# Optimization experiments

Measured on AMD Instinct MI355X. Metric: run time of the kernel, lower is better.

## Reference

```python
import jax, jax.numpy as jnp
import numpy as np
from jax import lax

Z_MAX = 0.3
WAVELENGTHS = jnp.array([0.65, 0.53, 0.47], jnp.float32)
LUMA = jnp.array([0.299, 0.587, 0.114], jnp.float32)


def conv2d(x, w, b):
    # x: (B,C,H,W), w: (O,I,kh,kw), SAME padding, stride 1
    y = lax.conv_general_dilated(x, w, (1, 1), 'SAME',
                                 dimension_numbers=('NCHW', 'OIHW', 'NCHW'))
    return y + b[None, :, None, None]


def group_norm(x, g, b, eps=1e-5):
    # GroupNorm(num_groups=1): normalize over (C,H,W) per sample
    mu = x.mean(axis=(1, 2, 3), keepdims=True)
    var = ((x - mu) ** 2).mean(axis=(1, 2, 3), keepdims=True)
    xn = (x - mu) * lax.rsqrt(var + eps)
    return xn * g[None, :, None, None] + b[None, :, None, None]


def setup_inputs() -> dict:
    key = jax.random.key(0)
    ks = jax.random.split(key, 16)
    B, C, H, W = 8, 3, 512, 512
    PH, ZH, MH = 16, 16, 32
    s = 0.1
    inp = {
        'x': jax.random.uniform(ks[0], (B, C, H, W), jnp.float32),
        'norm_g': jnp.ones((C,), jnp.float32), 'norm_b': jnp.zeros((C,), jnp.float32),
        'ph_w1': jax.random.normal(ks[1], (PH, C, 3, 3), jnp.float32) * s,
        'ph_b1': jnp.zeros((PH,), jnp.float32),
        'ph_w2': jax.random.normal(ks[2], (C, PH, 3, 3), jnp.float32) * s,
        'ph_b2': jnp.zeros((C,), jnp.float32),
        'z_w1': jax.random.normal(ks[3], (ZH, C, 3, 3), jnp.float32) * s,
        'z_b1': jnp.zeros((ZH,), jnp.float32),
        'z_w2': jax.random.normal(ks[4], (C, ZH, 3, 3), jnp.float32) * s,
        'z_b2': jnp.zeros((C,), jnp.float32),
        'freq_gain': jax.random.normal(ks[5], (C,), jnp.float32) * 0.01,
        'mix_w1': jax.random.normal(ks[6], (MH, C + 2, 3, 3), jnp.float32) * s,
        'mix_b1': jnp.zeros((MH,), jnp.float32),
        'gn1_g': jnp.ones((MH,), jnp.float32), 'gn1_b': jnp.zeros((MH,), jnp.float32),
        'mix_w2': jax.random.normal(ks[7], (MH, MH, 3, 3), jnp.float32) * s,
        'mix_b2': jnp.zeros((MH,), jnp.float32),
        'gn2_g': jnp.ones((MH,), jnp.float32), 'gn2_b': jnp.zeros((MH,), jnp.float32),
        'mix_w3': jax.random.normal(ks[8], (C, MH, 1, 1), jnp.float32) * s,
        'mix_b3': jnp.zeros((C,), jnp.float32),
        'se_w1': jax.random.normal(ks[9], (4, C), jnp.float32) * s,   # mid = max(3//4,4)=4
        'se_b1': jnp.zeros((4,), jnp.float32),
        'se_w2': jax.random.normal(ks[10], (C, 4), jnp.float32) * s,
        'se_b2': jnp.zeros((C,), jnp.float32),
        'alpha': jnp.asarray(0.3, jnp.float32),
    }
    return inp


def reference(x, norm_g, norm_b, ph_w1, ph_b1, ph_w2, ph_b2,
              z_w1, z_b1, z_w2, z_b2, freq_gain,
              mix_w1, mix_b1, gn1_g, gn1_b, mix_w2, mix_b2, gn2_g, gn2_b,
              mix_w3, mix_b3, se_w1, se_b1, se_w2, se_b2, alpha):
    B, C, H, W = x.shape
    # 1) norm
    xn = group_norm(x, norm_g, norm_b)
    # 2) phase prediction (small CNN, phi in [-pi, pi])
    h = jax.nn.silu(conv2d(xn, ph_w1, ph_b1))
    phi = jnp.tanh(conv2d(h, ph_w2, ph_b2)) * jnp.pi
    # 3) per-pixel propagation distance z in [0, z_max]
    hz = jax.nn.silu(conv2d(xn, z_w1, z_b1))
    z = jax.nn.sigmoid(conv2d(hz, z_w2, z_b2)) * Z_MAX
    # 4) complex field U0 = amp * exp(i*phi)  (amp_mode='identity')
    U0 = lax.complex(x * jnp.cos(phi), x * jnp.sin(phi))
    # 5) ASM propagation. kz = 2*pi*sqrt(1/lam^2 - fx^2 - fy^2), per-channel wavelength.
    fy = jnp.fft.fftfreq(H).astype(jnp.float32)
    fx = jnp.fft.fftfreq(W).astype(jnp.float32)
    f2 = fy[:, None] ** 2 + fx[None, :] ** 2                     # (H,W)
    inv_l2 = (1.0 / WAVELENGTHS ** 2)[:, None, None]             # (3,1,1)
    kz = 2.0 * jnp.pi * jnp.sqrt(jnp.maximum(inv_l2 - f2[None], 0.0))  # (3,H,W)
    # spatially varying z: base propagation at mean z + spatial phase correction
    z_mean = z.mean(axis=(2, 3), keepdims=True)                  # (B,3,1,1)
    Uf = jnp.fft.fft2(U0)
    Uf = Uf * (1.0 + freq_gain)[None, :, None, None].astype(Uf.dtype)  # FreqEnhance gain
    hp = kz[None] * z_mean                                       # (B,3,H,W)
    Uz = jnp.fft.ifft2(Uf * lax.complex(jnp.cos(hp), jnp.sin(hp)))
    k0 = (2.0 * jnp.pi / WAVELENGTHS)[None, :, None, None]
    cp = k0 * (z - z_mean)
    Uz = Uz * lax.complex(jnp.cos(cp), jnp.sin(cp))
    # 6) J = |Uz| with clamped sqrt
    J = jnp.sqrt(jnp.maximum(Uz.real ** 2 + Uz.imag ** 2, 1e-12))
    # 7) mix head: [x, J_luma, J_contrast] -> delta
    lw = LUMA[None, :, None, None]
    x_l = (x * lw).sum(axis=1, keepdims=True)
    J_l = (J * lw).sum(axis=1, keepdims=True)
    mix_in = jnp.concatenate([x, J_l, J_l - x_l], axis=1)        # (B,5,H,W)
    d = jax.nn.silu(group_norm(conv2d(mix_in, mix_w1, mix_b1), gn1_g, gn1_b))
    d = jax.nn.silu(group_norm(conv2d(d, mix_w2, mix_b2), gn2_g, gn2_b))
    delta = conv2d(d, mix_w3, mix_b3)                            # (B,3,H,W)
    # 8) SE channel attention
    p = delta.mean(axis=(2, 3))                                  # (B,3)
    wse = jax.nn.sigmoid(jax.nn.silu(p @ se_w1.T + se_b1) @ se_w2.T + se_b2)
    delta = delta * wse[:, :, None, None]
    # 9) residual update
    return x + alpha * delta
```

## Files before the change

kernel.cpp:

```cpp
#include <hip/hip_runtime.h>
#include <hip/hip_bf16.h>
#include <math.h>

#define DINL __device__ __forceinline__

namespace {
constexpr int Bn = 8, Cn = 3, Hn = 512, Wn = 512;
constexpr int HW  = Hn * Wn;
constexpr int CHW = Cn * HW;
constexpr float GEPS = 1e-5f;
constexpr float PIf  = 3.14159265358979323846f;

constexpr size_t OFF_RED = 0;
constexpr size_t OFF_PHI = 512;
constexpr size_t OFF_U   = OFF_PHI + (size_t)Bn * CHW * 2;
constexpr size_t OFF_J   = OFF_U   + (size_t)Bn * CHW * 4;
constexpr size_t OFF_D   = OFF_J   + (size_t)Bn * CHW * 2;
constexpr size_t OFF_Y2  = OFF_D   + (size_t)Bn * CHW * 2;
constexpr size_t OFF_W1B = OFF_Y2  + (size_t)Bn * 32 * HW;
constexpr size_t OFF_W2F = OFF_W1B + 3072 * 2;
constexpr size_t OFF_WH1 = OFF_W2F + 9216;
constexpr size_t OFF_WP2 = OFF_WH1 + 4608 * 2;
constexpr size_t OFF_WZ2 = OFF_WP2 + 4608;
constexpr size_t OFF_PRM = OFF_WZ2 + 4608;
constexpr size_t OFF_PART= OFF_PRM + 160 * 4;
constexpr int PZ = 0;
constexpr int PG1 = 24576;
constexpr int PG2 = 40960;
constexpr int PD  = 57344;
}

typedef __bf16 bfx8 __attribute__((ext_vector_type(8)));
typedef float  fx4  __attribute__((ext_vector_type(4)));

DINL float frcp(float a) { return __builtin_amdgcn_rcpf(a); }
DINL float sigm(float a) { return frcp(1.f + __expf(-a)); }
DINL float siluf(float a) { return a * frcp(1.f + __expf(-a)); }
DINL float ftanh(float a) { return 1.f - 2.f * frcp(1.f + __expf(2.f * a)); }
DINL unsigned short f2bf(float f) {
    unsigned u = __float_as_uint(f);
    return (unsigned short)((u + 0x7FFFu + ((u >> 16) & 1u)) >> 16);
}
DINL float bf2f(unsigned short h) {
    return __uint_as_float(((unsigned)h) << 16);
}
DINL unsigned short t1(float a) { return (unsigned short)(__float_as_uint(a) >> 16); }
DINL unsigned t2(float a, float b) {
    return (__float_as_uint(a) >> 16) | (__float_as_uint(b) & 0xFFFF0000u);
}
DINL unsigned char f2f8(float v) {
    return (unsigned char)(__builtin_amdgcn_cvt_pk_fp8_f32(v, v, 0, false) & 0xFF);
}
DINL unsigned short pk8(float a, float b) {
    return (unsigned short)(__builtin_amdgcn_cvt_pk_fp8_f32(a, b, 0, false) & 0xFFFF);
}
template<int SEL>
DINL float f8f(unsigned u) { return __builtin_amdgcn_cvt_f32_fp8(u, SEL); }
DINL unsigned pkh(float a, float b) {
    auto h = __builtin_amdgcn_cvt_pkrtz(a, b);
    unsigned u; __builtin_memcpy(&u, &h, 4); return u;
}
DINL float2 uph(unsigned u) {
    _Float16 h[2]; __builtin_memcpy(h, &u, 4);
    return make_float2((float)h[0], (float)h[1]);
}
DINL unsigned short f2h(float a) {
    _Float16 h = (_Float16)a; unsigned short s; __builtin_memcpy(&s, &h, 2); return s;
}
DINL float h2f(unsigned short s) {
    _Float16 h; __builtin_memcpy(&h, &s, 2); return (float)h;
}

DINL float blockReduceSum(float v) {
    __shared__ float sm[4];
    int lane = threadIdx.x & 63, wid = threadIdx.x >> 6;
    #pragma unroll
    for (int o = 32; o > 0; o >>= 1) v += __shfl_down(v, o, 64);
    __syncthreads();
    if (lane == 0) sm[wid] = v;
    __syncthreads();
    if (wid == 0) {
        float r = (lane < 4) ? sm[lane] : 0.f;
        r += __shfl_down(r, 2, 64);
        r += __shfl_down(r, 1, 64);
        return r;
    }
    return 0.f;
}

__global__ void k_zero(float* __restrict__ red) { red[threadIdx.x] = 0.f; }

__global__ __launch_bounds__(256) void k_red(const float* __restrict__ src,
                                             float* __restrict__ dst)
{
    const float4* s4 = (const float4*)(src + (size_t)blockIdx.x * 1024);
    float4 q = s4[threadIdx.x];
    float r = blockReduceSum(q.x + q.y + q.z + q.w);
    if (threadIdx.x == 0) dst[blockIdx.x] = r;
}

__global__ __launch_bounds__(256) void k_prep(
    const float* __restrict__ w1, const float* __restrict__ w2,
    const float* __restrict__ phw1, const float* __restrict__ zw1,
    const float* __restrict__ phw2, const float* __restrict__ zw2,
    const float* __restrict__ g2g, const float* __restrict__ g2b,
    const float* __restrict__ w3,
    unsigned short* __restrict__ w1bf, unsigned char* __restrict__ w2f8,
    unsigned short* __restrict__ wh1, unsigned char* __restrict__ wp2,
    unsigned char* __restrict__ wz2, float* __restrict__ prm)
{
    int i = blockIdx.x * 256 + threadIdx.x;
    if (i < 3072) {
        int o = i / 96, k = i - o * 96;
        int ky = k >> 5, r = k & 31, kx = r >> 3, c = r & 7;
        float v = (kx < 3 && c < 5) ? w1[o * 45 + c * 9 + ky * 3 + kx] : 0.f;
        w1bf[i] = f2bf(v);
    }
    if (i < 9216) {
        int tap = i >> 10, rr = i & 1023, o = rr >> 5, ci = rr & 31;
        w2f8[i] = f2f8(w2[o * 288 + ci * 9 + tap]);
    }
    if (i < 4608) {
        int o = i / 96, k = i - o * 96;
        int ky = k >> 5, r = k & 31, kx = r >> 3, c = r & 7;
        float v = 0.f;
        if (kx < 3 && c < 3)
            v = (o < 16) ? phw1[o * 27 + c * 9 + ky * 3 + kx]
                         : zw1[(o - 16) * 27 + c * 9 + ky * 3 + kx];
        wh1[i] = f2bf(v);
    }
    if (i < 4608) {
        int tap = i / 512, rr = i - tap * 512, n = rr >> 5, k = rr & 31;
        float vp = (n < 3 && k < 16) ? phw2[n * 144 + k * 9 + tap] : 0.f;
        float vz = (n < 3) ? zw2[n * 288 + k * 9 + tap] : 0.f;
        wp2[i] = f2f8(vp);
        wz2[i] = f2f8(vz);
    }
    if (i < 160) {
        if (i < 32) {
            int ch = (i & 1) * 16 + (i >> 1);
            prm[i] = g2g[ch];
        } else if (i < 64) {
            int j = i - 32, ch = (j & 1) * 16 + (j >> 1);
            prm[i] = g2b[ch];
        } else {
            int j = (i - 64) & 31, c = (i - 64) >> 5;
            int ch = (j & 1) * 16 + (j >> 1);
            prm[i] = w3[c * 32 + ch];
        }
    }
}

__global__ __launch_bounds__(256) void k_reduce_x(const float* __restrict__ x,
                                                  float* __restrict__ red) {
    int b = blockIdx.x >> 5, blk = blockIdx.x & 31;
    const float4* xv = (const float4*)(x + (size_t)b * CHW + (size_t)blk * (CHW / 32));
    float s = 0.f, ss = 0.f;
    for (int i = threadIdx.x; i < (CHW / 32) / 4; i += 256) {
        float4 v = xv[i];
        s  += v.x + v.y + v.z + v.w;
        ss += v.x * v.x + v.y * v.y + v.z * v.z + v.w * v.w;
    }
    float rs = blockReduceSum(s);
    float rss = blockReduceSum(ss);
    if (threadIdx.x == 0) { atomicAdd(&red[b], rs); atomicAdd(&red[8 + b], rss); }
}

__global__ __launch_bounds__(256) void k_heads(
    const float* __restrict__ x, const float* __restrict__ red,
    const float* __restrict__ ng, const float* __restrict__ nb,
    const unsigned short* __restrict__ wh1,
    const float* __restrict__ phb1, const float* __restrict__ zb1,
    const unsigned char* __restrict__ wp2, const unsigned char* __restrict__ wz2,
    const float* __restrict__ phb2, const float* __restrict__ zb2,
    unsigned short* __restrict__ phi, float* __restrict__ part)
{
    const int tx0 = blockIdx.x * 16, ty0 = blockIdx.y * 16, b = blockIdx.z;
    const int local = blockIdx.y * 32 + blockIdx.x;
    const bool edge = (blockIdx.x == 0) || (blockIdx.x == 31) ||
                      (blockIdx.y == 0) || (blockIdx.y == 31);
    __shared__ unsigned short mt8[20 * 21 * 8];
    __shared__ __attribute__((aligned(16))) unsigned char ht8[324 * 48];
    const int t = threadIdx.x;
    const float mu = red[b] * (1.f / CHW);
    const float rsv = rsqrtf(red[8 + b] * (1.f / CHW) - mu * mu + GEPS);
    float sc[3], sh[3];
    #pragma unroll
    for (int c = 0; c < 3; ++c) { sc[c] = rsv * ng[c]; sh[c] = nb[c] - mu * rsv * ng[c]; }
    if (edge) {
        for (int e = t; e < 20 * 21; e += 256) {
            int yy = e / 21, xx = e - yy * 21;
            int gy = ty0 - 2 + yy, gx = tx0 - 2 + xx;
            float v0 = 0, v1 = 0, v2 = 0;
            if (xx < 20 && (unsigned)gy < (unsigned)Hn && (unsigned)gx < (unsigned)Wn) {
                size_t p = (size_t)b * CHW + (size_t)gy * Wn + gx;
                v0 = x[p] * sc[0] + sh[0];
                v1 = x[p + HW] * sc[1] + sh[1];
                v2 = x[p + 2 * HW] * sc[2] + sh[2];
            }
            *(uint4*)(mt8 + e * 8) = make_uint4(t2(v0, v1), (unsigned)t1(v2), 0u, 0u);
        }
    } else {
        for (int e = t; e < 20 * 21; e += 256) {
            int yy = e / 21, xx = e - yy * 21;
            float v0 = 0, v1 = 0, v2 = 0;
            if (xx < 20) {
                size_t p = (size_t)b * CHW + (size_t)(ty0 - 2 + yy) * Wn + (tx0 - 2 + xx);
                v0 = x[p] * sc[0] + sh[0];
                v1 = x[p + HW] * sc[1] + sh[1];
                v2 = x[p + 2 * HW] * sc[2] + sh[2];
            }
            *(uint4*)(mt8 + e * 8) = make_uint4(t2(v0, v1), (unsigned)t1(v2), 0u, 0u);
        }
    }
    const int wv = t >> 6, lane = t & 63, ln = lane & 15, q = lane >> 4;
    bfx8 Bf[3][3];
    #pragma unroll
    for (int ks = 0; ks < 3; ++ks)
        #pragma unroll
        for (int nt = 0; nt < 3; ++nt)
            Bf[ks][nt] = *(const bfx8*)(wh1 + (nt * 16 + ln) * 96 + ks * 32 + q * 8);
    const float bb0 = phb1[ln], bb1 = zb1[ln], bb2 = zb1[16 + ln];
    __syncthreads();
    for (int mt = wv; mt < 21; mt += 4) {
        int p = mt * 16 + ln; if (p > 323) p = 323;
        const int hy = p / 18, hx = p - hy * 18;
        fx4 a0 = {0,0,0,0}, a1 = {0,0,0,0}, a2 = {0,0,0,0};
        #pragma unroll
        for (int ks = 0; ks < 3; ++ks) {
            bfx8 A = *(const bfx8*)(mt8 + ((hy + ks) * 21 + hx + q) * 8);
            a0 = __builtin_amdgcn_mfma_f32_16x16x32_bf16(A, Bf[ks][0], a0, 0, 0, 0);
            a1 = __builtin_amdgcn_mfma_f32_16x16x32_bf16(A, Bf[ks][1], a1, 0, 0, 0);
            a2 = __builtin_amdgcn_mfma_f32_16x16x32_bf16(A, Bf[ks][2], a2, 0, 0, 0);
        }
        const int prb = mt * 16 + q * 4;
        if (edge) {
            #pragma unroll
            for (int r = 0; r < 4; ++r) {
                const int pr = prb + r;
                if (pr < 324) {
                    const int py = pr / 18, px = pr - py * 18;
                    const int gy = ty0 - 1 + py, gx = tx0 - 1 + px;
                    const bool inimg = (unsigned)gy < (unsigned)Hn && (unsigned)gx < (unsigned)Wn;
                    unsigned char* hp = ht8 + pr * 48;
                    hp[ln]      = inimg ? f2f8(siluf(a0[r] + bb0)) : (unsigned char)0;
                    hp[16 + ln] = inimg ? f2f8(siluf(a1[r] + bb1)) : (unsigned char)0;
                    hp[32 + ln] = inimg ? f2f8(siluf(a2[r] + bb2)) : (unsigned char)0;
                }
            }
        } else {
            #pragma unroll
            for (int r = 0; r < 4; ++r) {
                const int pr = prb + r;
                if (pr < 324) {
                    unsigned char* hp = ht8 + pr * 48;
                    hp[ln]      = f2f8(siluf(a0[r] + bb0));
                    hp[16 + ln] = f2f8(siluf(a1[r] + bb1));
                    hp[32 + ln] = f2f8(siluf(a2[r] + bb2));
                }
            }
        }
    }
    __syncthreads();
    fx4 accp[4], accz[4];
    #pragma unroll
    for (int i = 0; i < 4; ++i) { accp[i] = fx4{0,0,0,0}; accz[i] = fx4{0,0,0,0}; }
    #pragma unroll
    for (int tap = 0; tap < 9; ++tap) {
        const int ky = tap / 3, kx = tap - ky * 3;
        long Bp = *(const long*)(wp2 + tap * 512 + ln * 32 + q * 8);
        long Bz = *(const long*)(wz2 + tap * 512 + ln * 32 + q * 8);
        #pragma unroll
        for (int i = 0; i < 4; ++i) {
            const int oy = wv * 4 + i;
            const unsigned char* ap = ht8 + ((oy + ky) * 18 + ln + kx) * 48;
            long Ap = *(const long*)(ap + q * 8);
            long Az = *(const long*)(ap + 16 + q * 8);
            accp[i] = __builtin_amdgcn_mfma_f32_16x16x32_fp8_fp8(Ap, Bp, accp[i], 0, 0, 0);
            accz[i] = __builtin_amdgcn_mfma_f32_16x16x32_fp8_fp8(Az, Bz, accz[i], 0, 0, 0);
        }
    }
    __syncthreads();
    float* phs = (float*)ht8;
    float* zs  = phs + 1024;
    if (ln < 3) {
        #pragma unroll
        for (int i = 0; i < 4; ++i)
            #pragma unroll
            for (int r = 0; r < 4; ++r) {
                int pl = (wv * 4 + i) * 16 + q * 4 + r;
                phs[pl * 4 + ln] = accp[i][r];
                zs [pl * 4 + ln] = accz[i][r];
            }
    }
    asm volatile("" ::: "memory");
    float4 pv = ((const float4*)phs)[t];
    float4 zv = ((const float4*)zs)[t];
    const int gy = ty0 + (t >> 4), gx = tx0 + (t & 15);
    size_t pp = (size_t)b * CHW + (size_t)gy * Wn + gx;
    phi[pp]          = f2h(ftanh(pv.x + phb2[0]) * PIf);
    phi[pp + HW]     = f2h(ftanh(pv.y + phb2[1]) * PIf);
    phi[pp + 2 * HW] = f2h(ftanh(pv.z + phb2[2]) * PIf);
    float z0 = sigm(zv.x + zb2[0]) * 0.3f;
    float z1 = sigm(zv.y + zb2[1]) * 0.3f;
    float z2 = sigm(zv.z + zb2[2]) * 0.3f;
    float r0 = blockReduceSum(z0);
    float r1 = blockReduceSum(z1);
    float r2 = blockReduceSum(z2);
    if (t == 0) {
        part[PZ + (size_t)(b * 3 + 0) * 1024 + local] = r0;
        part[PZ + (size_t)(b * 3 + 1) * 1024 + local] = r1;
        part[PZ + (size_t)(b * 3 + 2) * 1024 + local] = r2;
    }
}

template<bool INV>
DINL float2* fft512_wave4(float2* a, float2* b, const float2* tw, int l)
{
    float2* src = a; float2* dst = b;
    int s = 1;
    #pragma unroll
    for (int st = 0; st < 4; ++st) {
        #pragma unroll
        for (int h = 0; h < 2; ++h) {
            const int i = l + h * 64;
            const int q = i & (s - 1);
            const int sm = i - q;
            float2 A = src[i], B = src[i + 128], C = src[i + 256], D = src[i + 384];
            float t0x = A.x + C.x, t0y = A.y + C.y;
            float t1x = A.x - C.x, t1y = A.y - C.y;
            float t2x = B.x + D.x, t2y = B.y + D.y;
            float t3x = B.x - D.x, t3y = B.y - D.y;
            float i3x = INV ? -t3y : t3y;
            float i3y = INV ? t3x : -t3x;
            float u0x = t0x + t2x, u0y = t0y + t2y;
            float u2x = t0x - t2x, u2y = t0y - t2y;
            float u1x = t1x + i3x, u1y = t1y + i3y;
            float u3x = t1x - i3x, u3y = t1y - i3y;
            float2 w1 = tw[sm], w2 = tw[2 * sm], w3 = tw[3 * sm];
            float w1y = INV ? -w1.y : w1.y;
            float w2y = INV ? -w2.y : w2.y;
            float w3y = INV ? -w3.y : w3.y;
            const int base = q + 4 * sm;
            dst[base]         = make_float2(u0x, u0y);
            dst[base + s]     = make_float2(u1x * w1.x - u1y * w1y, u1x * w1y + u1y * w1.x);
// ... 57 lines not shown
    __shared__ unsigned ta[32][33];
    __shared__ unsigned tb[32][33];
    const int t = threadIdx.x;
    const int cc = t & 31, r0 = t >> 5;
    const int ar = ti * 32, ac = tj * 32;
    #pragma unroll
    for (int k = 0; k < 4; ++k) {
        int r = r0 + k * 8;
        ta[r][cc] = Ub[(size_t)(ar + r) * 512 + ac + cc];
    }
    if (ti != tj) {
        #pragma unroll
        for (int k = 0; k < 4; ++k) {
            int r = r0 + k * 8;
            tb[r][cc] = Ub[(size_t)(ac + r) * 512 + ar + cc];
        }
    }
    __syncthreads();
    #pragma unroll
    for (int k = 0; k < 4; ++k) {
        int r = r0 + k * 8;
        Ub[(size_t)(ac + r) * 512 + ar + cc] = ta[cc][r];
    }
    if (ti != tj) {
        #pragma unroll
        for (int k = 0; k < 4; ++k) {
            int r = r0 + k * 8;
            Ub[(size_t)(ar + r) * 512 + ac + cc] = tb[cc][r];
        }
    }
}

__global__ __launch_bounds__(256) void k_fftB(
    unsigned* __restrict__ U, const float* __restrict__ red, const float* __restrict__ fgain)
{
    __shared__ float2 buf[4][2][512];
    __shared__ float2 tw[512];
    const int t = threadIdx.x, wv = t >> 6, l = t & 63;
    #pragma unroll
    for (int i = t; i < 512; i += 256) {
        float s, c; __sincosf(-2.f * PIf * (float)i * (1.f / 512.f), &s, &c);
        tw[i] = make_float2(c, s);
    }
    __syncthreads();
    const int line = blockIdx.x * 4 + wv;
    const int bc = line >> 9;
    const int fw = line & 511;
    const int c = bc % 3;
    unsigned* Ur = U + (size_t)line * 512;
    float2* A = buf[wv][0];
    float2* B = buf[wv][1];
    #pragma unroll
    for (int i = l; i < 512; i += 64) A[i] = uph(Ur[i]);
    asm volatile("" ::: "memory");
    float2* res = fft512_wave4<false>(A, B, tw, l);
    const float zm   = red[16 + bc] * (1.f / HW);
    const float gain = 1.f + fgain[c];
    const float lam  = (c == 0) ? 0.65f : (c == 1) ? 0.53f : 0.47f;
    const float il2  = 1.f / (lam * lam);
    const float fwv  = (float)(fw < 256 ? fw : fw - 512) * (1.f / 512.f);
    const float f2w  = fwv * fwv;
    #pragma unroll
    for (int i = l; i < 512; i += 64) {
        float fh = (float)(i < 256 ? i : i - 512) * (1.f / 512.f);
        float kz = 2.f * PIf * sqrtf(fmaxf(il2 - f2w - fh * fh, 0.f));
        float sn, cs; __sincosf(kz * zm, &sn, &cs);
        float2 v = res[i];
        res[i] = make_float2(gain * (v.x * cs - v.y * sn), gain * (v.x * sn + v.y * cs));
    }
    asm volatile("" ::: "memory");
    float2* other = (res == A) ? B : A;
    float2* res2 = fft512_wave4<true>(res, other, tw, l);
    #pragma unroll
    for (int i = l; i < 512; i += 64) {
        float2 v = res2[i];
        Ur[i] = pkh(v.x * (1.f / 512.f), v.y * (1.f / 512.f));
    }
}

__global__ __launch_bounds__(256) void k_fftC(
    const unsigned* __restrict__ U, unsigned short* __restrict__ J)
{
    __shared__ float2 buf[4][2][512];
    __shared__ float2 tw[512];
    const int t = threadIdx.x, wv = t >> 6, l = t & 63;
    #pragma unroll
    for (int i = t; i < 512; i += 256) {
        float s, c; __sincosf(-2.f * PIf * (float)i * (1.f / 512.f), &s, &c);
        tw[i] = make_float2(c, s);
// ... 52 lines not shown
        for (int nt = 0; nt < 2; ++nt)
            Bf[ks][nt] = *(const bfx8*)(w1bf + (nt * 16 + ln) * 96 + ks * 32 + q * 8);
    const float b1v0 = b1[ln], b1v1 = b1[16 + ln];
    float s = 0.f, ss = 0.f;
    #pragma unroll
    for (int i = 0; i < 4; ++i) {
        const int oy = wv * 4 + i;
        fx4 a0 = {0.f, 0.f, 0.f, 0.f}, a1 = {0.f, 0.f, 0.f, 0.f};
        #pragma unroll
        for (int ks = 0; ks < 3; ++ks) {
            bfx8 A = *(const bfx8*)(mt8 + ((oy + ks) * 19 + ln + q) * 8);
            a0 = __builtin_amdgcn_mfma_f32_16x16x32_bf16(A, Bf[ks][0], a0, 0, 0, 0);
            a1 = __builtin_amdgcn_mfma_f32_16x16x32_bf16(A, Bf[ks][1], a1, 0, 0, 0);
        }
        #pragma unroll
        for (int r = 0; r < 4; ++r) {
            float u0 = a0[r] + b1v0, u1 = a1[r] + b1v1;
            s += u0 + u1; ss += u0 * u0 + u1 * u1;
        }
    }
    float rs = blockReduceSum(s);
    float rss = blockReduceSum(ss);
    if (t == 0) {
        part[PG1 + (size_t)b * 1024 + local] = rs;
        part[PG1 + (size_t)(8 + b) * 1024 + local] = rss;
    }
}

__global__ __launch_bounds__(256) void k_m2(
    const float* __restrict__ x, const unsigned short* __restrict__ Jb,
    const unsigned short* __restrict__ w1bf, const float* __restrict__ b1,
    const float* __restrict__ g1g, const float* __restrict__ g1b,
    const unsigned char* __restrict__ w2f8, const float* __restrict__ b2,
    const float* __restrict__ red, float* __restrict__ part,
    unsigned char* __restrict__ y2)
{
    const int tx0 = blockIdx.x * 16, ty0 = blockIdx.y * 16, b = blockIdx.z;
    const int local = blockIdx.y * 32 + blockIdx.x;
    const bool edge = (blockIdx.x == 0) || (blockIdx.x == 31) ||
                      (blockIdx.y == 0) || (blockIdx.y == 31);
    __shared__ unsigned short mt8[20 * 21 * 8];
    __shared__ __attribute__((aligned(16))) unsigned char dt2[324 * 40];
    const int t = threadIdx.x;
    const float mu1 = red[40 + b] * (1.f / (32.f * HW));
    const float rs1 = rsqrtf(red[48 + b] * (1.f / (32.f * HW)) - mu1 * mu1 + GEPS);
    for (int e = t; e < 20 * 21; e += 256) {
        int yy = e / 21, xx = e - yy * 21;
        int gy = ty0 - 2 + yy, gx = tx0 - 2 + xx;
        float v0 = 0, v1 = 0, v2 = 0, jl = 0, d5 = 0;
        bool ok = edge ? (xx < 20 && (unsigned)gy < (unsigned)Hn && (unsigned)gx < (unsigned)Wn)
                       : (xx < 20);
        if (ok) {
            size_t p = (size_t)b * CHW + (size_t)gy * Wn + gx;
            v0 = x[p]; v1 = x[p + HW]; v2 = x[p + 2 * HW];
            float j0 = h2f(Jb[p]), j1 = h2f(Jb[p + HW]), j2 = h2f(Jb[p + 2 * HW]);
            float xl = 0.299f * v0 + 0.587f * v1 + 0.114f * v2;
            jl = 0.299f * j0 + 0.587f * j1 + 0.114f * j2;
            d5 = jl - xl;
        }
        *(uint4*)(mt8 + e * 8) = make_uint4(t2(v0, v1), t2(v2, jl), (unsigned)t1(d5), 0u);
    }
    const int wv = t >> 6, lane = t & 63, ln = lane & 15, q = lane >> 4;
    const float sc0 = rs1 * g1g[ln],       sc1 = rs1 * g1g[16 + ln];
    const float of0 = (b1[ln] - mu1) * sc0 + g1b[ln];
    const float of1 = (b1[16 + ln] - mu1) * sc1 + g1b[16 + ln];
    bfx8 Bf[3][2];
    #pragma unroll
    for (int ks = 0; ks < 3; ++ks)
        #pragma unroll
        for (int nt = 0; nt < 2; ++nt)
            Bf[ks][nt] = *(const bfx8*)(w1bf + (nt * 16 + ln) * 96 + ks * 32 + q * 8);
    __syncthreads();
    for (int mt = wv; mt < 21; mt += 4) {
        int p = mt * 16 + ln; if (p > 323) p = 323;
        const int hy = p / 18, hx = p - hy * 18;
        fx4 a0 = {0.f, 0.f, 0.f, 0.f}, a1 = {0.f, 0.f, 0.f, 0.f};
        #pragma unroll
        for (int ks = 0; ks < 3; ++ks) {
            bfx8 A = *(const bfx8*)(mt8 + ((hy + ks) * 21 + hx + q) * 8);
            a0 = __builtin_amdgcn_mfma_f32_16x16x32_bf16(A, Bf[ks][0], a0, 0, 0, 0);
            a1 = __builtin_amdgcn_mfma_f32_16x16x32_bf16(A, Bf[ks][1], a1, 0, 0, 0);
        }
        const int prb = mt * 16 + q * 4;
        if (edge) {
            #pragma unroll
            for (int r = 0; r < 4; ++r) {
                const int pr = prb + r;
                if (pr < 324) {
                    const int py = pr / 18, px = pr - py * 18;
                    const int gy = ty0 - 1 + py, gx = tx0 - 1 + px;
                    const bool inimg = (unsigned)gy < (unsigned)Hn && (unsigned)gx < (unsigned)Wn;
                    dt2[pr * 40 + ln]      = inimg ? f2f8(siluf(a0[r] * sc0 + of0)) : (unsigned char)0;
                    dt2[pr * 40 + 16 + ln] = inimg ? f2f8(siluf(a1[r] * sc1 + of1)) : (unsigned char)0;
                }
            }
        } else {
            #pragma unroll
            for (int r = 0; r < 4; ++r) {
                const int pr = prb + r;
                if (pr < 324) {
                    dt2[pr * 40 + ln]      = f2f8(siluf(a0[r] * sc0 + of0));
                    dt2[pr * 40 + 16 + ln] = f2f8(siluf(a1[r] * sc1 + of1));
                }
            }
        }
    }
    __syncthreads();
    fx4 c2[4][2];
    #pragma unroll
    for (int i = 0; i < 4; ++i)
        #pragma unroll
        for (int nt = 0; nt < 2; ++nt)
            c2[i][nt] = fx4{0.f, 0.f, 0.f, 0.f};
    #pragma unroll
    for (int tap = 0; tap < 9; ++tap) {
        const int ky = tap / 3, kx = tap - ky * 3;
        long B0 = *(const long*)(w2f8 + tap * 1024 + ln * 32 + q * 8);
        long B1 = *(const long*)(w2f8 + tap * 1024 + (16 + ln) * 32 + q * 8);
        #pragma unroll
        for (int i = 0; i < 4; ++i) {
            const int oy = wv * 4 + i;
            long A = *(const long*)(dt2 + ((oy + ky) * 18 + ln + kx) * 40 + q * 8);
            c2[i][0] = __builtin_amdgcn_mfma_f32_16x16x32_fp8_fp8(A, B0, c2[i][0], 0, 0, 0);
            c2[i][1] = __builtin_amdgcn_mfma_f32_16x16x32_fp8_fp8(A, B1, c2[i][1], 0, 0, 0);
        }
    }
    float s = 0.f, ss = 0.f;
    const float b2v0 = b2[ln], b2v1 = b2[16 + ln];
    #pragma unroll
    for (int i = 0; i < 4; ++i) {
        const int gy = ty0 + wv * 4 + i;
        #pragma unroll
        for (int r = 0; r < 4; ++r) {
            const int gx = tx0 + q * 4 + r;
            float a0 = c2[i][0][r] + b2v0;
            float a1 = c2[i][1][r] + b2v1;
            s += a0 + a1; ss += a0 * a0 + a1 * a1;
            size_t off = ((size_t)b * HW + (size_t)gy * Wn + gx) * 32 + ln * 2;
            *(unsigned short*)(y2 + off) = pk8(a0, a1);
        }
    }
    float rsum = blockReduceSum(s);
    float rss = blockReduceSum(ss);
    if (t == 0) {
        part[PG2 + (size_t)b * 1024 + local] = rsum;
        part[PG2 + (size_t)(8 + b) * 1024 + local] = rss;
    }
}

__global__ __launch_bounds__(256) void k_m3(
    const unsigned char* __restrict__ y2, const float* __restrict__ red,
    const float* __restrict__ prm, const float* __restrict__ b3,
    unsigned short* __restrict__ dl, float* __restrict__ part)
{
    int idx = blockIdx.x * 256 + threadIdx.x;
    int b = idx >> 18;
    int pix = idx & (HW - 1);
    const int local = blockIdx.x & 1023;
    float mu = red[56 + b] * (1.f / (32.f * HW));
    float rs = rsqrtf(red[64 + b] * (1.f / (32.f * HW)) - mu * mu + GEPS);
    const uint4* yp = (const uint4*)(y2 + (size_t)idx * 32);
    uint4 L0 = yp[0], L1 = yp[1];
    unsigned Lw[8] = {L0.x, L0.y, L0.z, L0.w, L1.x, L1.y, L1.z, L1.w};
    float a0 = b3[0], a1 = b3[1], a2 = b3[2];
    #pragma unroll
    for (int w = 0; w < 8; ++w) {
        unsigned u = Lw[w];
        float vv[4] = { f8f<0>(u), f8f<1>(u), f8f<2>(u), f8f<3>(u) };
        #pragma unroll
        for (int h = 0; h < 4; ++h) {
            int j = w * 4 + h;
            float dn = (vv[h] - mu) * rs * prm[j] + prm[32 + j];
            float sv = siluf(dn);
            a0 += sv * prm[64 + j]; a1 += sv * prm[96 + j]; a2 += sv * prm[128 + j];
        }
    }
    size_t p = (size_t)b * CHW + pix;
    dl[p] = f2h(a0); dl[p + HW] = f2h(a1); dl[p + 2 * HW] = f2h(a2);
    float r0 = blockReduceSum(a0);
    float r1 = blockReduceSum(a1);
    float r2 = blockReduceSum(a2);
    if (threadIdx.x == 0) {
        part[PD + (size_t)(b * 3 + 0) * 1024 + local] = r0;
        part[PD + (size_t)(b * 3 + 1) * 1024 + local] = r1;
        part[PD + (size_t)(b * 3 + 2) * 1024 + local] = r2;
    }
}

__global__ void k_se(float* __restrict__ red,
    const float* __restrict__ w1, const float* __restrict__ b1,
    const float* __restrict__ w2, const float* __restrict__ b2,
    const float* __restrict__ alpha)
{
    int b = threadIdx.x;
    if (b < 8) {
        float p0 = red[72 + b * 3 + 0] * (1.f / HW);
        float p1 = red[72 + b * 3 + 1] * (1.f / HW);
        float p2 = red[72 + b * 3 + 2] * (1.f / HW);
        float h[4];
        #pragma unroll
        for (int j = 0; j < 4; ++j) {
            float a = b1[j] + p0 * w1[j * 3] + p1 * w1[j * 3 + 1] + p2 * w1[j * 3 + 2];
            h[j] = siluf(a);
        }
        float al = alpha[0];
        #pragma unroll
        for (int c = 0; c < 3; ++c) {
            float a = b2[c] + h[0] * w2[c * 4] + h[1] * w2[c * 4 + 1]
                            + h[2] * w2[c * 4 + 2] + h[3] * w2[c * 4 + 3];
            red[96 + b * 3 + c] = al * sigm(a);
        }
    }
}

__global__ __launch_bounds__(256) void k_out(
    const float* __restrict__ x, const unsigned short* __restrict__ dl,
    const float* __restrict__ red, float* __restrict__ out)
{
// ... 27 lines not shown
    const float* fgain = (const float*)d_in[11];
    const float* mw1   = (const float*)d_in[12];
    const float* mb1   = (const float*)d_in[13];
    const float* g1g   = (const float*)d_in[14];
    const float* g1b   = (const float*)d_in[15];
    const float* mw2   = (const float*)d_in[16];
    const float* mb2   = (const float*)d_in[17];
    const float* g2g   = (const float*)d_in[18];
    const float* g2b   = (const float*)d_in[19];
    const float* mw3   = (const float*)d_in[20];
    const float* mb3   = (const float*)d_in[21];
    const float* sw1   = (const float*)d_in[22];
    const float* sb1   = (const float*)d_in[23];
    const float* sw2   = (const float*)d_in[24];
    const float* sb2   = (const float*)d_in[25];
    const float* alpha = (const float*)d_in[26];

    char* ws = (char*)d_ws;
    float*  red = (float*)(ws + OFF_RED);
    unsigned short* phi = (unsigned short*)(ws + OFF_PHI);
    unsigned* U = (unsigned*)(ws + OFF_U);
    unsigned short* Jb = (unsigned short*)(ws + OFF_J);
    unsigned short* dl = (unsigned short*)(ws + OFF_D);
    unsigned char*  y2   = (unsigned char*)(ws + OFF_Y2);
    unsigned short* w1bf = (unsigned short*)(ws + OFF_W1B);
    unsigned char*  w2f8 = (unsigned char*)(ws + OFF_W2F);
    unsigned short* wh1  = (unsigned short*)(ws + OFF_WH1);
    unsigned char*  wp2  = (unsigned char*)(ws + OFF_WP2);
    unsigned char*  wz2  = (unsigned char*)(ws + OFF_WZ2);
    float* prm  = (float*)(ws + OFF_PRM);
    float* part = (float*)(ws + OFF_PART);
    float* out = (float*)d_out;

    hipLaunchKernelGGL(k_zero, dim3(1), dim3(128), 0, stream, red);
    hipLaunchKernelGGL(k_prep, dim3(36), dim3(256), 0, stream,
                       mw1, mw2, ph_w1, z_w1, ph_w2, z_w2, g2g, g2b, mw3,
                       w1bf, w2f8, wh1, wp2, wz2, prm);
    hipLaunchKernelGGL(k_reduce_x, dim3(256), dim3(256), 0, stream, x, red);
    hipLaunchKernelGGL(k_heads, dim3(32, 32, 8), dim3(256), 0, stream,
                       x, red, ng, nb, wh1, ph_b1, z_b1, wp2, wz2, ph_b2, z_b2, phi, part);
    hipLaunchKernelGGL(k_red, dim3(24), dim3(256), 0, stream, part + PZ, red + 16);
    hipLaunchKernelGGL(k_fftA, dim3(3072), dim3(256), 0, stream, x, phi, U);
    hipLaunchKernelGGL(k_transpose, dim3(136, 24), dim3(256), 0, stream, U);
    hipLaunchKernelGGL(k_fftB, dim3(3072), dim3(256), 0, stream, U, red, fgain);
    hipLaunchKernelGGL(k_transpose, dim3(136, 24), dim3(256), 0, stream, U);
    hipLaunchKernelGGL(k_fftC, dim3(3072), dim3(256), 0, stream, U, Jb);
    hipLaunchKernelGGL(k_m1, dim3(32, 32, 8), dim3(256), 0, stream, x, Jb, w1bf, mb1, part);
    hipLaunchKernelGGL(k_red, dim3(16), dim3(256), 0, stream, part + PG1, red + 40);
    hipLaunchKernelGGL(k_m2, dim3(32, 32, 8), dim3(256), 0, stream,
                       x, Jb, w1bf, mb1, g1g, g1b, w2f8, mb2, red, part, y2);
    hipLaunchKernelGGL(k_red, dim3(16), dim3(256), 0, stream, part + PG2, red + 56);
    hipLaunchKernelGGL(k_m3, dim3(8192), dim3(256), 0, stream, y2, red, prm, mb3, dl, part);
    hipLaunchKernelGGL(k_red, dim3(24), dim3(256), 0, stream, part + PD, red + 72);
    hipLaunchKernelGGL(k_se, dim3(1), dim3(64), 0, stream, red, sw1, sb1, sw2, sb2, alpha);
    hipLaunchKernelGGL(k_out, dim3(6144), dim3(256), 0, stream, x, dl, red, out);
}
```

Measured before the change: 499.9 us.

## Fold small reduction kernels into consumers and pack MFMA epilogue stores

Merges the zero, weight-prep and x-statistics kernels into one launch and removes the separate k_red passes, so each consumer (heads, fftB, m2, m3) reduces its partial sums from the part buffer at block start. The MFMA operand order is swapped so each lane holds four channels of one pixel, which lets the silu/fp8 epilogue pack four values and store one 32-bit word instead of individual bytes. Three-way block reductions are fused into one pass, and the m3 fp8 unpack uses the packed convert builtin. This cuts launch count and scalar LDS traffic, at the cost of redundant partial-sum reductions repeated in every block.

Measured after the change: 469.0 us. 6.2% less time.

```diff
diff --git a/kernel.cpp b/kernel.cpp
--- a/kernel.cpp
+++ b/kernel.cpp
@@ -32,6 +32,7 @@
 
 typedef __bf16 bfx8 __attribute__((ext_vector_type(8)));
 typedef float  fx4  __attribute__((ext_vector_type(4)));
+typedef float  fx2  __attribute__((ext_vector_type(2)));
 
 DINL float frcp(float a) { return __builtin_amdgcn_rcpf(a); }
 DINL float sigm(float a) { return frcp(1.f + __expf(-a)); }
@@ -54,6 +55,11 @@
 DINL unsigned short pk8(float a, float b) {
     return (unsigned short)(__builtin_amdgcn_cvt_pk_fp8_f32(a, b, 0, false) & 0xFFFF);
 }
+DINL unsigned pk4f8(float a, float b, float c, float d) {
+    unsigned u = __builtin_amdgcn_cvt_pk_fp8_f32(a, b, 0, false);
+    u = __builtin_amdgcn_cvt_pk_fp8_f32(c, d, u, true);
+    return u;
+}
 template<int SEL>
 DINL float f8f(unsigned u) { return __builtin_amdgcn_cvt_f32_fp8(u, SEL); }
 DINL unsigned pkh(float a, float b) {
@@ -88,7 +94,24 @@
     return 0.f;
 }
 
-__global__ void k_zero(float* __restrict__ red) { red[threadIdx.x] = 0.f; }
+DINL void blockReduceSum3(float& a, float& b, float& c) {
+    __shared__ float sm3[12];
+    int lane = threadIdx.x & 63, wid = threadIdx.x >> 6;
+    #pragma unroll
+    for (int o = 32; o > 0; o >>= 1) {
+        a += __shfl_down(a, o, 64);
+        b += __shfl_down(b, o, 64);
+        c += __shfl_down(c, o, 64);
+    }
+    __syncthreads();
+    if (lane == 0) { sm3[wid] = a; sm3[4 + wid] = b; sm3[8 + wid] = c; }
+    __syncthreads();
+    if (threadIdx.x == 0) {
+        a = sm3[0] + sm3[1] + sm3[2] + sm3[3];
+        b = sm3[4] + sm3[5] + sm3[6] + sm3[7];
+        c = sm3[8] + sm3[9] + sm3[10] + sm3[11];
+    }
+}
 
 __global__ __launch_bounds__(256) void k_red(const float* __restrict__ src,
                                              float* __restrict__ dst)
@@ -99,7 +122,7 @@
     if (threadIdx.x == 0) dst[blockIdx.x] = r;
 }
 
-__global__ __launch_bounds__(256) void k_prep(
+__global__ __launch_bounds__(256) void k_init(
     const float* __restrict__ w1, const float* __restrict__ w2,
     const float* __restrict__ phw1, const float* __restrict__ zw1,
     const float* __restrict__ phw2, const float* __restrict__ zw2,
@@ -107,53 +130,54 @@
     const float* __restrict__ w3,
     unsigned short* __restrict__ w1bf, unsigned char* __restrict__ w2f8,
     unsigned short* __restrict__ wh1, unsigned char* __restrict__ wp2,
-    unsigned char* __restrict__ wz2, float* __restrict__ prm)
-{
-    int i = blockIdx.x * 256 + threadIdx.x;
-    if (i < 3072) {
-        int o = i / 96, k = i - o * 96;
-        int ky = k >> 5, r = k & 31, kx = r >> 3, c = r & 7;
-        float v = (kx < 3 && c < 5) ? w1[o * 45 + c * 9 + ky * 3 + kx] : 0.f;
-        w1bf[i] = f2bf(v);
-    }
-    if (i < 9216) {
-        int tap = i >> 10, rr = i & 1023, o = rr >> 5, ci = rr & 31;
-        w2f8[i] = f2f8(w2[o * 288 + ci * 9 + tap]);
-    }
-    if (i < 4608) {
-        int o = i / 96, k = i - o * 96;
-        int ky = k >> 5, r = k & 31, kx = r >> 3, c = r & 7;
-        float v = 0.f;
-        if (kx < 3 && c < 3)
-            v = (o < 16) ? phw1[o * 27 + c * 9 + ky * 3 + kx]
-                         : zw1[(o - 16) * 27 + c * 9 + ky * 3 + kx];
-        wh1[i] = f2bf(v);
-    }
-    if (i < 4608) {
-        int tap = i / 512, rr = i - tap * 512, n = rr >> 5, k = rr & 31;
-        float vp = (n < 3 && k < 16) ? phw2[n * 144 + k * 9 + tap] : 0.f;
-        float vz = (n < 3) ? zw2[n * 288 + k * 9 + tap] : 0.f;
-        wp2[i] = f2f8(vp);
-        wz2[i] = f2f8(vz);
-    }
-    if (i < 160) {
-        if (i < 32) {
-            int ch = (i & 1) * 16 + (i >> 1);
-            prm[i] = g2g[ch];
-        } else if (i < 64) {
-            int j = i - 32, ch = (j & 1) * 16 + (j >> 1);
-            prm[i] = g2b[ch];
-        } else {
-            int j = (i - 64) & 31, c = (i - 64) >> 5;
-            int ch = (j & 1) * 16 + (j >> 1);
-            prm[i] = w3[c * 32 + ch];
-        }
-    }
-}
-
-__global__ __launch_bounds__(256) void k_reduce_x(const float* __restrict__ x,
-                                                  float* __restrict__ red) {
-    int b = blockIdx.x >> 5, blk = blockIdx.x & 31;
+    unsigned char* __restrict__ wz2, float* __restrict__ prm,
+    const float* __restrict__ x, float* __restrict__ part)
+{
+    if (blockIdx.x < 36) {
+        int i = blockIdx.x * 256 + threadIdx.x;
+        if (i < 3072) {
+            int o = i / 96, k = i - o * 96;
+            int ky = k >> 5, r = k & 31, kx = r >> 3, c = r & 7;
+            float v = (kx < 3 && c < 5) ? w1[o * 45 + c * 9 + ky * 3 + kx] : 0.f;
+            w1bf[i] = f2bf(v);
+        }
+        if (i < 9216) {
+            int tap = i >> 10, rr = i & 1023, o = rr >> 5, ci = rr & 31;
+            w2f8[i] = f2f8(w2[o * 288 + ci * 9 + tap]);
+        }
+        if (i < 4608) {
+            int o = i / 96, k = i - o * 96;
+            int ky = k >> 5, r = k & 31, kx = r >> 3, c = r & 7;
+            float v = 0.f;
+            if (kx < 3 && c < 3)
+                v = (o < 16) ? phw1[o * 27 + c * 9 + ky * 3 + kx]
+                             : zw1[(o - 16) * 27 + c * 9 + ky * 3 + kx];
+            wh1[i] = f2bf(v);
+        }
+        if (i < 4608) {
+            int tap = i / 512, rr = i - tap * 512, n = rr >> 5, k = rr & 31;
+            float vp = (n < 3 && k < 16) ? phw2[n * 144 + k * 9 + tap] : 0.f;
+            float vz = (n < 3) ? zw2[n * 288 + k * 9 + tap] : 0.f;
+            wp2[i] = f2f8(vp);
+            wz2[i] = f2f8(vz);
+        }
+        if (i < 160) {
+            if (i < 32) {
+                int ch = (i & 1) * 16 + (i >> 1);
+                prm[i] = g2g[ch];
+            } else if (i < 64) {
+                int j = i - 32, ch = (j & 1) * 16 + (j >> 1);
+                prm[i] = g2b[ch];
+            } else {
+                int j = (i - 64) & 31, c = (i - 64) >> 5;
+                int ch = (j & 1) * 16 + (j >> 1);
+                prm[i] = w3[c * 32 + ch];
+            }
+        }
+        return;
+    }
+    const int bid = blockIdx.x - 36;
+    const int b = bid >> 5, blk = bid & 31;
     const float4* xv = (const float4*)(x + (size_t)b * CHW + (size_t)blk * (CHW / 32));
     float s = 0.f, ss = 0.f;
     for (int i = threadIdx.x; i < (CHW / 32) / 4; i += 256) {
@@ -163,11 +187,14 @@
     }
     float rs = blockReduceSum(s);
     float rss = blockReduceSum(ss);
-    if (threadIdx.x == 0) { atomicAdd(&red[b], rs); atomicAdd(&red[8 + b], rss); }
+    if (threadIdx.x == 0) {
+        part[PG1 + b * 64 + blk] = rs;
+        part[PG1 + b * 64 + 32 + blk] = rss;
+    }
 }
 
 __global__ __launch_bounds__(256) void k_heads(
-    const float* __restrict__ x, const float* __restrict__ red,
+    const float* __restrict__ x,
     const float* __restrict__ ng, const float* __restrict__ nb,
     const unsigned short* __restrict__ wh1,
     const float* __restrict__ phb1, const float* __restrict__ zb1,
@@ -181,9 +208,19 @@
                       (blockIdx.y == 0) || (blockIdx.y == 31);
     __shared__ unsigned short mt8[20 * 21 * 8];
     __shared__ __attribute__((aligned(16))) unsigned char ht8[324 * 48];
+    __shared__ float xst[2];
     const int t = threadIdx.x;
-    const float mu = red[b] * (1.f / CHW);
-    const float rsv = rsqrtf(red[8 + b] * (1.f / CHW) - mu * mu + GEPS);
+    {
+        const float* px = part + PG1 + (size_t)b * 64;
+        float sv  = (t < 32) ? px[t] : 0.f;
+        float ssv = (t >= 32 && t < 64) ? px[t] : 0.f;
+        float r0 = blockReduceSum(sv);
+        float r1 = blockReduceSum(ssv);
+        if (t == 0) { xst[0] = r0; xst[1] = r1; }
+        __syncthreads();
+    }
+    const float mu = xst[0] * (1.f / CHW);
+    const float rsv = rsqrtf(xst[1] * (1.f / CHW) - mu * mu + GEPS);
     float sc[3], sh[3];
     #pragma unroll
     for (int c = 0; c < 3; ++c) { sc[c] = rsv * ng[c]; sh[c] = nb[c] - mu * rsv * ng[c]; }
@@ -220,7 +257,12 @@
         #pragma unroll
         for (int nt = 0; nt < 3; ++nt)
             Bf[ks][nt] = *(const bfx8*)(wh1 + (nt * 16 + ln) * 96 + ks * 32 + q * 8);
-    const float bb0 = phb1[ln], bb1 = zb1[ln], bb2 = zb1[16 + ln];
+    float bph[4], bz0[4], bz1[4];
+    #pragma unroll
+    for (int r = 0; r < 4; ++r) {
+        int ch = q * 4 + r;
+        bph[r] = phb1[ch]; bz0[r] = zb1[ch]; bz1[r] = zb1[16 + ch];
+    }
     __syncthreads();
     for (int mt = wv; mt < 21; mt += 4) {
         int p = mt * 16 + ln; if (p > 323) p = 323;
@@ -229,37 +271,24 @@
         #pragma unroll
         for (int ks = 0; ks < 3; ++ks) {
             bfx8 A = *(const bfx8*)(mt8 + ((hy + ks) * 21 + hx + q) * 8);
-            a0 = __builtin_amdgcn_mfma_f32_16x16x32_bf16(A, Bf[ks][0], a0, 0, 0, 0);
-            a1 = __builtin_amdgcn_mfma_f32_16x16x32_bf16(A, Bf[ks][1], a1, 0, 0, 0);
-            a2 = __builtin_amdgcn_mfma_f32_16x16x32_bf16(A, Bf[ks][2], a2, 0, 0, 0);
-        }
-        const int prb = mt * 16 + q * 4;
+            a0 = __builtin_amdgcn_mfma_f32_16x16x32_bf16(Bf[ks][0], A, a0, 0, 0, 0);
+            a1 = __builtin_amdgcn_mfma_f32_16x16x32_bf16(Bf[ks][1], A, a1, 0, 0, 0);
+            a2 = __builtin_amdgcn_mfma_f32_16x16x32_bf16(Bf[ks][2], A, a2, 0, 0, 0);
+        }
+        bool live = true;
         if (edge) {
-            #pragma unroll
-            for (int r = 0; r < 4; ++r) {
-                const int pr = prb + r;
-                if (pr < 324) {
-                    const int py = pr / 18, px = pr - py * 18;
-                    const int gy = ty0 - 1 + py, gx = tx0 - 1 + px;
-                    const bool inimg = (unsigned)gy < (unsigned)Hn && (unsigned)gx < (unsigned)Wn;
-                    unsigned char* hp = ht8 + pr * 48;
-                    hp[ln]      = inimg ? f2f8(siluf(a0[r] + bb0)) : (unsigned char)0;
-                    hp[16 + ln] = inimg ? f2f8(siluf(a1[r] + bb1)) : (unsigned char)0;
-                    hp[32 + ln] = inimg ? f2f8(siluf(a2[r] + bb2)) : (unsigned char)0;
-                }
-            }
-        } else {
-            #pragma unroll
-            for (int r = 0; r < 4; ++r) {
-                const int pr = prb + r;
-                if (pr < 324) {
-                    unsigned char* hp = ht8 + pr * 48;
-                    hp[ln]      = f2f8(siluf(a0[r] + bb0));
-                    hp[16 + ln] = f2f8(siluf(a1[r] + bb1));
-                    hp[32 + ln] = f2f8(siluf(a2[r] + bb2));
-                }
-            }
-        }
+            const int gy = ty0 - 1 + hy, gx = tx0 - 1 + hx;
+            live = (unsigned)gy < (unsigned)Hn && (unsigned)gx < (unsigned)Wn;
+        }
+        unsigned d0 = pk4f8(siluf(a0[0] + bph[0]), siluf(a0[1] + bph[1]),
+                            siluf(a0[2] + bph[2]), siluf(a0[3] + bph[3]));
+        unsigned d1 = pk4f8(siluf(a1[0] + bz0[0]), siluf(a1[1] + bz0[1]),
+                            siluf(a1[2] + bz0[2]), siluf(a1[3] + bz0[3]));
+        unsigned d2 = pk4f8(siluf(a2[0] + bz1[0]), siluf(a2[1] + bz1[1]),
+                            siluf(a2[2] + bz1[2]), siluf(a2[3] + bz1[3]));
+        if (!live) { d0 = 0u; d1 = 0u; d2 = 0u; }
+        unsigned* hp = (unsigned*)(ht8 + p * 48 + q * 4);
+        hp[0] = d0; hp[4] = d1; hp[8] = d2;
     }
     __syncthreads();
     fx4 accp[4], accz[4];
@@ -304,13 +333,11 @@
     float z0 = sigm(zv.x + zb2[0]) * 0.3f;
     float z1 = sigm(zv.y + zb2[1]) * 0.3f;
     float z2 = sigm(zv.z + zb2[2]) * 0.3f;
-    float r0 = blockReduceSum(z0);
-    float r1 = blockReduceSum(z1);
-    float r2 = blockReduceSum(z2);
+    blockReduceSum3(z0, z1, z2);
     if (t == 0) {
-        part[PZ + (size_t)(b * 3 + 0) * 1024 + local] = r0;
-        part[PZ + (size_t)(b * 3 + 1) * 1024 + local] = r1;
-        part[PZ + (size_t)(b * 3 + 2) * 1024 + local] = r2;
+        part[PZ + (size_t)(b * 3 + 0) * 1024 + local] = z0;
+        part[PZ + (size_t)(b * 3 + 1) * 1024 + local] = z1;
+        part[PZ + (size_t)(b * 3 + 2) * 1024 + local] = z2;
     }
 }
 
@@ -434,15 +461,22 @@
 }
 
 __global__ __launch_bounds__(256) void k_fftB(
-    unsigned* __restrict__ U, const float* __restrict__ red, const float* __restrict__ fgain)
+    unsigned* __restrict__ U, const float* __restrict__ part, const float* __restrict__ fgain)
 {
     __shared__ float2 buf[4][2][512];
     __shared__ float2 tw[512];
+    __shared__ float zmS;
     const int t = threadIdx.x, wv = t >> 6, l = t & 63;
     #pragma unroll
     for (int i = t; i < 512; i += 256) {
         float s, c; __sincosf(-2.f * PIf * (float)i * (1.f / 512.f), &s, &c);
         tw[i] = make_float2(c, s);
+    }
+    const int bc0 = (blockIdx.x * 4) >> 9;
+    {
+        float4 a4 = ((const float4*)(part + PZ + (size_t)bc0 * 1024))[t];
+        float r = blockReduceSum(a4.x + a4.y + a4.z + a4.w);
+        if (t == 0) zmS = r * (1.f / HW);
     }
     __syncthreads();
     const int line = blockIdx.x * 4 + wv;
@@ -456,7 +490,7 @@
     for (int i = l; i < 512; i += 64) A[i] = uph(Ur[i]);
     asm volatile("" ::: "memory");
     float2* res = fft512_wave4<false>(A, B, tw, l);
-    const float zm   = red[16 + bc] * (1.f / HW);
+    const float zm   = zmS;
     const float gain = 1.f + fgain[c];
     const float lam  = (c == 0) ? 0.65f : (c == 1) ? 0.53f : 0.47f;
     const float il2  = 1.f / (lam * lam);
@@ -575,8 +609,7 @@
     const unsigned short* __restrict__ w1bf, const float* __restrict__ b1,
     const float* __restrict__ g1g, const float* __restrict__ g1b,
     const unsigned char* __restrict__ w2f8, const float* __restrict__ b2,
-    const float* __restrict__ red, float* __restrict__ part,
-    unsigned char* __restrict__ y2)
+    float* __restrict__ part, unsigned char* __restrict__ y2)
 {
     const int tx0 = blockIdx.x * 16, ty0 = blockIdx.y * 16, b = blockIdx.z;
     const int local = blockIdx.y * 32 + blockIdx.x;
@@ -584,9 +617,18 @@
                       (blockIdx.y == 0) || (blockIdx.y == 31);
     __shared__ unsigned short mt8[20 * 21 * 8];
     __shared__ __attribute__((aligned(16))) unsigned char dt2[324 * 40];
+    __shared__ float g1s[2];
     const int t = threadIdx.x;
-    const float mu1 = red[40 + b] * (1.f / (32.f * HW));
-    const float rs1 = rsqrtf(red[48 + b] * (1.f / (32.f * HW)) - mu1 * mu1 + GEPS);
+    {
+        float4 a4 = ((const float4*)(part + PG1 + (size_t)b * 1024))[t];
+        float4 c4 = ((const float4*)(part + PG1 + (size_t)(8 + b) * 1024))[t];
+        float r0 = blockReduceSum(a4.x + a4.y + a4.z + a4.w);
+        float r1 = blockReduceSum(c4.x + c4.y + c4.z + c4.w);
+        if (t == 0) { g1s[0] = r0; g1s[1] = r1; }
+        __syncthreads();
+    }
+    const float mu1 = g1s[0] * (1.f / (32.f * HW));
+    const float rs1 = rsqrtf(g1s[1] * (1.f / (32.f * HW)) - mu1 * mu1 + GEPS);
     for (int e = t; e < 20 * 21; e += 256) {
         int yy = e / 21, xx = e - yy * 21;
         int gy = ty0 - 2 + yy, gx = tx0 - 2 + xx;
@@ -604,9 +646,16 @@
         *(uint4*)(mt8 + e * 8) = make_uint4(t2(v0, v1), t2(v2, jl), (unsigned)t1(d5), 0u);
     }
     const int wv = t >> 6, lane = t & 63, ln = lane & 15, q = lane >> 4;
-    const float sc0 = rs1 * g1g[ln],       sc1 = rs1 * g1g[16 + ln];
-    const float of0 = (b1[ln] - mu1) * sc0 + g1b[ln];
-    const float of1 = (b1[16 + ln] - mu1) * sc1 + g1b[16 + ln];
+    float scv[2][4], ofv[2][4];
+    #pragma unroll
+    for (int g = 0; g < 2; ++g)
+        #pragma unroll
+        for (int r = 0; r < 4; ++r) {
+            int ch = g * 16 + q * 4 + r;
+            float sg = rs1 * g1g[ch];
+            scv[g][r] = sg;
+            ofv[g][r] = (b1[ch] - mu1) * sg + g1b[ch];
+        }
     bfx8 Bf[3][2];
     #pragma unroll
     for (int ks = 0; ks < 3; ++ks)
@@ -621,32 +670,25 @@
         #pragma unroll
         for (int ks = 0; ks < 3; ++ks) {
             bfx8 A = *(const bfx8*)(mt8 + ((hy + ks) * 21 + hx + q) * 8);
-            a0 = __builtin_amdgcn_mfma_f32_16x16x32_bf16(A, Bf[ks][0], a0, 0, 0, 0);
-            a1 = __builtin_amdgcn_mfma_f32_16x16x32_bf16(A, Bf[ks][1], a1, 0, 0, 0);
-        }
-        const int prb = mt * 16 + q * 4;
+            a0 = __builtin_amdgcn_mfma_f32_16x16x32_bf16(Bf[ks][0], A, a0, 0, 0, 0);
+            a1 = __builtin_amdgcn_mfma_f32_16x16x32_bf16(Bf[ks][1], A, a1, 0, 0, 0);
+        }
+        bool live = true;
         if (edge) {
-            #pragma unroll
-            for (int r = 0; r < 4; ++r) {
-                const int pr = prb + r;
-                if (pr < 324) {
-                    const int py = pr / 18, px = pr - py * 18;
-                    const int gy = ty0 - 1 + py, gx = tx0 - 1 + px;
-                    const bool inimg = (unsigned)gy < (unsigned)Hn && (unsigned)gx < (unsigned)Wn;
-                    dt2[pr * 40 + ln]      = inimg ? f2f8(siluf(a0[r] * sc0 + of0)) : (unsigned char)0;
-                    dt2[pr * 40 + 16 + ln] = inimg ? f2f8(siluf(a1[r] * sc1 + of1)) : (unsigned char)0;
-                }
-            }
-        } else {
-            #pragma unroll
-            for (int r = 0; r < 4; ++r) {
-                const int pr = prb + r;
-                if (pr < 324) {
-                    dt2[pr * 40 + ln]      = f2f8(siluf(a0[r] * sc0 + of0));
-                    dt2[pr * 40 + 16 + ln] = f2f8(siluf(a1[r] * sc1 + of1));
-                }
-            }
-        }
+            const int gy = ty0 - 1 + hy, gx = tx0 - 1 + hx;
+            live = (unsigned)gy < (unsigned)Hn && (unsigned)gx < (unsigned)Wn;
+        }
+        unsigned d0 = pk4f8(siluf(a0[0] * scv[0][0] + ofv[0][0]),
+                            siluf(a0[1] * scv[0][1] + ofv[0][1]),
+                            siluf(a0[2] * scv[0][2] + ofv[0][2]),
+                            siluf(a0[3] * scv[0][3] + ofv[0][3]));
+        unsigned d1 = pk4f8(siluf(a1[0] * scv[1][0] + ofv[1][0]),
+                            siluf(a1[1] * scv[1][1] + ofv[1][1]),
+                            siluf(a1[2] * scv[1][2] + ofv[1][2]),
+                            siluf(a1[3] * scv[1][3] + ofv[1][3]));
+        if (!live) { d0 = 0u; d1 = 0u; }
+        unsigned* dp = (unsigned*)(dt2 + p * 40 + q * 4);
+        dp[0] = d0; dp[4] = d1;
     }
     __syncthreads();
     fx4 c2[4][2];
@@ -692,16 +734,26 @@
 }
 
 __global__ __launch_bounds__(256) void k_m3(
-    const unsigned char* __restrict__ y2, const float* __restrict__ red,
+    const unsigned char* __restrict__ y2,
     const float* __restrict__ prm, const float* __restrict__ b3,
     unsigned short* __restrict__ dl, float* __restrict__ part)
 {
-    int idx = blockIdx.x * 256 + threadIdx.x;
-    int b = idx >> 18;
+    const int t = threadIdx.x;
+    const int b = blockIdx.x >> 10;
+    __shared__ float g2s[2];
+    {
+        float4 a4 = ((const float4*)(part + PG2 + (size_t)b * 1024))[t];
+        float4 c4 = ((const float4*)(part + PG2 + (size_t)(8 + b) * 1024))[t];
+        float r0 = blockReduceSum(a4.x + a4.y + a4.z + a4.w);
+        float r1 = blockReduceSum(c4.x + c4.y + c4.z + c4.w);
+        if (t == 0) { g2s[0] = r0; g2s[1] = r1; }
+        __syncthreads();
+    }
+    const float mu = g2s[0] * (1.f / (32.f * HW));
+    const float rs = rsqrtf(g2s[1] * (1.f / (32.f * HW)) - mu * mu + GEPS);
+    int idx = blockIdx.x * 256 + t;
     int pix = idx & (HW - 1);
     const int local = blockIdx.x & 1023;
-    float mu = red[56 + b] * (1.f / (32.f * HW));
-    float rs = rsqrtf(red[64 + b] * (1.f / (32.f * HW)) - mu * mu + GEPS);
     const uint4* yp = (const uint4*)(y2 + (size_t)idx * 32);
     uint4 L0 = yp[0], L1 = yp[1];
     unsigned Lw[8] = {L0.x, L0.y, L0.z, L0.w, L1.x, L1.y, L1.z, L1.w};
@@ -709,7 +761,13 @@
     #pragma unroll
     for (int w = 0; w < 8; ++w) {
         unsigned u = Lw[w];
+#if __has_builtin(__builtin_amdgcn_cvt_pk_f32_fp8)
+        fx2 lo = __builtin_amdgcn_cvt_pk_f32_fp8(u, false);
+        fx2 hi = __builtin_amdgcn_cvt_pk_f32_fp8(u, true);
+        float vv[4] = { lo[0], lo[1], hi[0], hi[1] };
+#else
         float vv[4] = { f8f<0>(u), f8f<1>(u), f8f<2>(u), f8f<3>(u) };
+#endif
         #pragma unroll
         for (int h = 0; h < 4; ++h) {
             int j = w * 4 + h;
@@ -720,13 +778,11 @@
     }
     size_t p = (size_t)b * CHW + pix;
     dl[p] = f2h(a0); dl[p + HW] = f2h(a1); dl[p + 2 * HW] = f2h(a2);
-    float r0 = blockReduceSum(a0);
-    float r1 = blockReduceSum(a1);
-    float r2 = blockReduceSum(a2);
-    if (threadIdx.x == 0) {
-        part[PD + (size_t)(b * 3 + 0) * 1024 + local] = r0;
-        part[PD + (size_t)(b * 3 + 1) * 1024 + local] = r1;
-        part[PD + (size_t)(b * 3 + 2) * 1024 + local] = r2;
+    blockReduceSum3(a0, a1, a2);
+    if (t == 0) {
+        part[PD + (size_t)(b * 3 + 0) * 1024 + local] = a0;
+        part[PD + (size_t)(b * 3 + 1) * 1024 + local] = a1;
+        part[PD + (size_t)(b * 3 + 2) * 1024 + local] = a2;
     }
 }
 
@@ -820,25 +876,20 @@
     float* part = (float*)(ws + OFF_PART);
     float* out = (float*)d_out;
 
-    hipLaunchKernelGGL(k_zero, dim3(1), dim3(128), 0, stream, red);
-    hipLaunchKernelGGL(k_prep, dim3(36), dim3(256), 0, stream,
+    hipLaunchKernelGGL(k_init, dim3(292), dim3(256), 0, stream,
                        mw1, mw2, ph_w1, z_w1, ph_w2, z_w2, g2g, g2b, mw3,
-                       w1bf, w2f8, wh1, wp2, wz2, prm);
-    hipLaunchKernelGGL(k_reduce_x, dim3(256), dim3(256), 0, stream, x, red);
+                       w1bf, w2f8, wh1, wp2, wz2, prm, x, part);
     hipLaunchKernelGGL(k_heads, dim3(32, 32, 8), dim3(256), 0, stream,
-                       x, red, ng, nb, wh1, ph_b1, z_b1, wp2, wz2, ph_b2, z_b2, phi, part);
-    hipLaunchKernelGGL(k_red, dim3(24), dim3(256), 0, stream, part + PZ, red + 16);
+                       x, ng, nb, wh1, ph_b1, z_b1, wp2, wz2, ph_b2, z_b2, phi, part);
     hipLaunchKernelGGL(k_fftA, dim3(3072), dim3(256), 0, stream, x, phi, U);
     hipLaunchKernelGGL(k_transpose, dim3(136, 24), dim3(256), 0, stream, U);
-    hipLaunchKernelGGL(k_fftB, dim3(3072), dim3(256), 0, stream, U, red, fgain);
+    hipLaunchKernelGGL(k_fftB, dim3(3072), dim3(256), 0, stream, U, part, fgain);
     hipLaunchKernelGGL(k_transpose, dim3(136, 24), dim3(256), 0, stream, U);
     hipLaunchKernelGGL(k_fftC, dim3(3072), dim3(256), 0, stream, U, Jb);
     hipLaunchKernelGGL(k_m1, dim3(32, 32, 8), dim3(256), 0, stream, x, Jb, w1bf, mb1, part);
-    hipLaunchKernelGGL(k_red, dim3(16), dim3(256), 0, stream, part + PG1, red + 40);
     hipLaunchKernelGGL(k_m2, dim3(32, 32, 8), dim3(256), 0, stream,
-                       x, Jb, w1bf, mb1, g1g, g1b, w2f8, mb2, red, part, y2);
-    hipLaunchKernelGGL(k_red, dim3(16), dim3(256), 0, stream, part + PG2, red + 56);
-    hipLaunchKernelGGL(k_m3, dim3(8192), dim3(256), 0, stream, y2, red, prm, mb3, dl, part);
+                       x, Jb, w1bf, mb1, g1g, g1b, w2f8, mb2, part, y2);
+    hipLaunchKernelGGL(k_m3, dim3(8192), dim3(256), 0, stream, y2, prm, mb3, dl, part);
     hipLaunchKernelGGL(k_red, dim3(24), dim3(256), 0, stream, part + PD, red + 72);
     hipLaunchKernelGGL(k_se, dim3(1), dim3(64), 0, stream, red, sw1, sb1, sw2, sb2, alpha);
     hipLaunchKernelGGL(k_out, dim3(6144), dim3(256), 0, stream, x, dl, red, out);
```
